# Kernel tuning notes

Measured on AMD Instinct MI355X. Metric: run time of the kernel, lower is better.

Reference implementation:

```python
import jax, jax.numpy as jnp
import numpy as np

B, D, H, O = 4096, 1024, 8192, 1000

def _l2norm_rows(w):
    return w / jnp.maximum(jnp.linalg.norm(w, axis=1, keepdims=True), 1e-12)

def setup_inputs() -> dict:
    key = jax.random.key(0)
    k1, k2, k3 = jax.random.split(key, 3)
    x = jax.random.normal(k1, (B, D), dtype=jnp.float32)
    kohonen_weights = _l2norm_rows(jax.random.normal(k2, (H, D), dtype=jnp.float32))
    grossberg_weights = _l2norm_rows(jax.random.normal(k3, (O, H), dtype=jnp.float32))
    return {"x": x, "kohonen_weights": kohonen_weights, "grossberg_weights": grossberg_weights}

def reference(x, kohonen_weights, grossberg_weights):
    # x: [B, D] (already flat), kohonen_weights: [H, D], grossberg_weights: [O, H]
    x2 = jnp.sum(x * x, axis=1, keepdims=True)              # [B, 1]
    w2 = jnp.sum(kohonen_weights * kohonen_weights, axis=1)  # [H]
    # Euclidean cdist via the expanded quadratic form (same as torch.cdist p=2)
    sq = x2 + w2[None, :] - 2.0 * (x @ kohonen_weights.T)    # [B, H]
    distances = jnp.sqrt(jnp.maximum(sq, 0.0))
    winners = jnp.argmin(distances, axis=1)                  # [B] int
    # one_hot @ grossberg_weights.T is exactly a row gather of grossberg_weights.T
    output = jnp.take(grossberg_weights.T, winners, axis=0)  # [B, O]
    return (output, winners)
```

## Files before the change

### kernel.cpp

```cpp
#include <hip/hip_runtime.h>
#include <hip/hip_bf16.h>
#include <hip/hip_fp16.h>


#define BB 4096
#define DD 1024
#define HH 8192
#define OO 1000

#define BM 128
#define BN 128
#define BK 64
#define NITER (DD / BK)
#define NTILES (HH / BN)
#define SA_TILE (BM * BK)
#define SB_TILE (BN * BK)

typedef _Float16 f16;
typedef float f32x16 __attribute__((ext_vector_type(16)));
typedef int v8i __attribute__((ext_vector_type(8)));
typedef int v4i __attribute__((ext_vector_type(4)));
union Frag { v8i v; v4i h[2]; };

typedef __attribute__((address_space(3))) uint32_t lds_u32_t;
typedef __attribute__((address_space(1))) uint32_t glb_u32_t;

__device__ __forceinline__ uint32_t packkey(float v, int col) {
  uint32_t u = __float_as_uint(v);
  uint32_t mask = (uint32_t)((int32_t)u >> 31) | 0x80000000u;
  u ^= mask;
  return (u & 0xFFFFFF80u) | (uint32_t)col;
}
__device__ __forceinline__ float unpackval(uint32_t k) {
  uint32_t u = k & 0xFFFFFF80u;
  uint32_t mask = (k & 0x80000000u) ? 0x80000000u : 0xFFFFFFFFu;
  return __uint_as_float(u ^ mask);
}
__device__ __forceinline__ void kmerge(uint32_t& k1, uint32_t& k2,
                                       uint32_t o1, uint32_t o2) {
  uint32_t mn = min(k1, o1);
  uint32_t alt = (k1 > o1) ? k2 : o2;
  k1 = max(k1, o1);
  k2 = max(mn, alt);
}

__global__ __launch_bounds__(256) void cvt_kernel(
    const float* __restrict__ x, const float* __restrict__ kw,
    uint8_t* __restrict__ xq, uint8_t* __restrict__ kq,
    const float* __restrict__ G, float* __restrict__ Gt) {
  const int tid = threadIdx.x;
  const int blk = blockIdx.x;
  __shared__ float tile[32][33];
  if (blk < (BB + HH) / 4) {
#pragma unroll
    for (int i = 0; i < 4; ++i) {
      int r = blk * 4 + i;
      const float* src = (r < BB) ? (x + (size_t)r * DD)
                                  : (kw + (size_t)(r - BB) * DD);
      uint8_t* dst = (r < BB) ? (xq + (size_t)r * DD)
                              : (kq + (size_t)(r - BB) * DD);
      float4 v = ((const float4*)src)[tid];
      int p = 0;
      p = __builtin_amdgcn_cvt_pk_fp8_f32(v.x, v.y, p, false);
      p = __builtin_amdgcn_cvt_pk_fp8_f32(v.z, v.w, p, true);
      ((int*)dst)[tid] = p;
    }
  } else {
    if (Gt == nullptr) return;
    const int tb = blk - (BB + HH) / 4;
    const int tx = tid & 31;
    const int ty = tid >> 5;
#pragma unroll 1
    for (int j4 = 0; j4 < 4; ++j4) {
      int tile_id = tb * 4 + j4;
      int h0 = (tile_id >> 5) * 32;
      int o0 = (tile_id & 31) * 32;
      __syncthreads();
#pragma unroll
      for (int j = 0; j < 4; ++j) {
        int o = o0 + ty + j * 8;
        if (o < OO) tile[ty + j * 8][tx] = G[(size_t)o * HH + h0 + tx];
      }
      __syncthreads();
#pragma unroll
      for (int j = 0; j < 4; ++j) {
        int o = o0 + tx;
        int h = h0 + ty + j * 8;
        if (o < OO) Gt[(size_t)h * OO + o] = tile[tx][ty + j * 8];
      }
    }
  }
}

__global__ __launch_bounds__(256, 3) void gemm_top2(
    const uint8_t* __restrict__ A, const uint8_t* __restrict__ Bt,
    uint4* __restrict__ pk) {
  __shared__ __align__(16) uint8_t sA[2][SA_TILE];
  __shared__ __align__(16) uint8_t sB[2][SB_TILE];
  __shared__ uint2 mk[BM][2];

  const int tid = threadIdx.x;
  const int w = tid >> 6;
  const int L = tid & 63;

  const int bid = blockIdx.y * gridDim.x + blockIdx.x;
  const int c8 = bid & 7;
  const int tt = bid >> 3;
  const int nx = c8 * 8 + (tt & 7);
  const int my = tt >> 3;
  const int m0 = my * BM;
  const int n0 = nx * BN;

  const int wr = w >> 1;
  const int wc = w & 1;

  f32x16 acc[2][2];
#pragma unroll
  for (int i = 0; i < 2; ++i)
#pragma unroll
    for (int j = 0; j < 2; ++j)
#pragma unroll
      for (int q = 0; q < 16; ++q) acc[i][j][q] = 0.f;

  const int l31 = L & 31;
  const int kh = L >> 5;

  const uint8_t* pA[2]; int dA[2];
  const uint8_t* pB[2]; int dB[2];
#pragma unroll
  for (int j = 0; j < 2; ++j) {
    int c = tid + 256 * j;
    int r = c >> 2;
    int so = ((c & 3) ^ ((r >> 1) & 3)) * 16;
    pA[j] = A + (size_t)(m0 + r) * DD + so;
    pB[j] = Bt + (size_t)(n0 + r) * DD + so;
    dA[j] = c * 16;
    dB[j] = c * 16;
  }

  auto stage = [&](int t, int p) {
#pragma unroll
    for (int j = 0; j < 2; ++j)
      __builtin_amdgcn_global_load_lds((const glb_u32_t*)(pA[j] + (size_t)t * BK),
                                       (lds_u32_t*)(&sA[p][0] + dA[j]), 16, 0, 0);
#pragma unroll
    for (int j = 0; j < 2; ++j)
      __builtin_amdgcn_global_load_lds((const glb_u32_t*)(pB[j] + (size_t)t * BK),
                                       (lds_u32_t*)(&sB[p][0] + dB[j]), 16, 0, 0);
  };

  const int t2 = (l31 >> 1) & 3;
  const int off_lo = ((2 * kh) ^ t2) * 16;
  const int off_hi = ((2 * kh + 1) ^ t2) * 16;
  const int raBase = (wr * 64 + l31) * BK;
  const int rbBase = (wc * 64 + l31) * BK;

  stage(0, 0);

#pragma unroll 1
  for (int kt = 0; kt < NITER; ++kt) {
    asm volatile("s_waitcnt lgkmcnt(0)" ::: "memory");
    __builtin_amdgcn_s_barrier();
    asm volatile("" ::: "memory");

    if (kt < NITER - 1) {
      stage(kt + 1, (kt + 1) & 1);
      asm volatile("s_waitcnt vmcnt(4)" ::: "memory");
    } else {
      asm volatile("s_waitcnt vmcnt(0)" ::: "memory");
    }

    const uint8_t* bufA = &sA[kt & 1][0];
    const uint8_t* bufB = &sB[kt & 1][0];

    __builtin_amdgcn_s_setprio(1);
    Frag af[2], bf[2];
#pragma unroll
    for (int j = 0; j < 2; ++j) {
      const uint8_t* base = bufA + raBase + j * 32 * BK;
      af[j].h[0] = *(const v4i*)(base + off_lo);
      af[j].h[1] = *(const v4i*)(base + off_hi);
    }
#pragma unroll
    for (int i = 0; i < 2; ++i) {
      const uint8_t* base = bufB + rbBase + i * 32 * BK;
      bf[i].h[0] = *(const v4i*)(base + off_lo);
      bf[i].h[1] = *(const v4i*)(base + off_hi);
    }
#pragma unroll
    for (int i = 0; i < 2; ++i)
#pragma unroll
      for (int j = 0; j < 2; ++j)
        acc[i][j] = __builtin_amdgcn_mfma_scale_f32_32x32x64_f8f6f4(
            bf[i].v, af[j].v, acc[i][j],
            0 , 0 ,
            0, 0x7F7F7F7Fu , 0, 0x7F7F7F7Fu);
    __builtin_amdgcn_s_setprio(0);
  }

#pragma unroll
  for (int j = 0; j < 2; ++j) {
    uint32_t k1 = 0, k2 = 0;
#pragma unroll
    for (int i = 0; i < 2; ++i) {
#pragma unroll
      for (int q = 0; q < 16; ++q) {
        int hcol = wc * 64 + i * 32 + (q & 3) + 8 * (q >> 2) + 4 * kh;
        uint32_t kj = packkey(acc[i][j][q], hcol);
        if (kj > k1) { k2 = k1; k1 = kj; }
        else k2 = max(k2, kj);
      }
    }
    uint32_t o1 = (uint32_t)__shfl_xor((int)k1, 32, 64);
    uint32_t o2 = (uint32_t)__shfl_xor((int)k2, 32, 64);
    kmerge(k1, k2, o1, o2);
    if (kh == 0) mk[wr * 64 + j * 32 + l31][wc] = make_uint2(k1, k2);
  }
  __syncthreads();
  if (tid < BM) {
    uint2 a = mk[tid][0], b = mk[tid][1];
    pk[(size_t)(m0 + tid) * NTILES + nx] = make_uint4(a.x, a.y, b.x, b.y);
  }
}

__global__ __launch_bounds__(256) void select_kernel(
    const float* __restrict__ x, const float* __restrict__ kw,
    const uint4* __restrict__ pk,
    const float* __restrict__ Gt, const float* __restrict__ G,
    float* __restrict__ out, float* __restrict__ out_w) {
  const int b = blockIdx.x * 4 + (threadIdx.x >> 6);
  const int L = threadIdx.x & 63;

  const float4* x4 = (const float4*)(x + (size_t)b * DD);
  float4 xv[4];
#pragma unroll
  for (int j = 0; j < 4; ++j) xv[j] = x4[L + 64 * j];

  uint4 kp = pk[(size_t)b * NTILES + L];

  double x2 = 0.0;
#pragma unroll
  for (int j = 0; j < 4; ++j)
    x2 += (double)xv[j].x * xv[j].x + (double)xv[j].y * xv[j].y +
          (double)xv[j].z * xv[j].z + (double)xv[j].w * xv[j].w;
#pragma unroll
  for (int msk = 1; msk < 64; msk <<= 1) x2 += __shfl_xor(x2, msk, 64);

  uint32_t m = max(kp.x, kp.z);
#pragma unroll
  for (int msk = 1; msk < 64; msk <<= 1)
    m = max(m, (uint32_t)__shfl_xor((int)m, msk, 64));
  const uint32_t thrk = packkey(unpackval(m) - 0.35f, 0);

  unsigned long long cand[4];
  cand[0] = __ballot(kp.x >= thrk);
  cand[1] = __ballot(kp.y >= thrk);
  cand[2] = __ballot(kp.z >= thrk);
  cand[3] = __ballot(kp.w >= thrk);

  double best = 1e300;
  int bestc = 0x7fffffff;
#pragma unroll 1
  for (int pass = 0; pass < 4; ++pass) {
    unsigned long long bits = cand[pass];
    uint32_t mykey = (pass == 0) ? kp.x : (pass == 1) ? kp.y
                    : (pass == 2) ? kp.z : kp.w;
    while (bits) {
      int tt = __ffsll((long long)bits) - 1;
      bits &= bits - 1;
      uint32_t kbt = (uint32_t)__shfl((int)mykey, tt, 64);
      int col = tt * 128 + (int)(kbt & 127u);
      const float4* k4 = (const float4*)(kw + (size_t)col * DD);
      double dot = 0.0, w2 = 0.0;
#pragma unroll
      for (int j = 0; j < 4; ++j) {
        float4 wv = k4[L + 64 * j];
        dot += (double)xv[j].x * wv.x + (double)xv[j].y * wv.y +
               (double)xv[j].z * wv.z + (double)xv[j].w * wv.w;
        w2 += (double)wv.x * wv.x + (double)wv.y * wv.y +
              (double)wv.z * wv.z + (double)wv.w * wv.w;
      }
#pragma unroll
      for (int msk = 1; msk < 64; msk <<= 1) {
        dot += __shfl_xor(dot, msk, 64);
        w2 += __shfl_xor(w2, msk, 64);
      }
      double sq = x2 + w2 - 2.0 * dot;
      if (sq < best || (sq == best && col < bestc)) { best = sq; bestc = col; }
    }
  }

  if (L == 0) out_w[b] = (float)bestc;
  if (Gt != nullptr) {
    const float4* gsrc = (const float4*)(Gt + (size_t)bestc * OO);
    float4* gdst = (float4*)(out + (size_t)b * OO);
#pragma unroll
    for (int j = 0; j < 4; ++j) {
      int q = L + 64 * j;
      if (q < OO / 4) gdst[q] = gsrc[q];
    }
  } else {
#pragma unroll 1
    for (int j = 0; j < 16; ++j) {
      int o = L + 64 * j;
      if (o < OO) out[(size_t)b * OO + o] = G[(size_t)o * HH + bestc];
    }
  }
}

extern "C" void kernel_launch(void* const* d_in, const int* in_sizes, int n_in,
                              void* d_out, int out_size, void* d_ws, size_t ws_size,
                              hipStream_t stream) {
  const float* x  = (const float*)d_in[0];
  const float* kw = (const float*)d_in[1];
  const float* gw = (const float*)d_in[2];
  float* out = (float*)d_out;
  float* out_w = out + (size_t)BB * OO;

  const size_t MB = 1024 * 1024;
  char* ws = (char*)d_ws;
  uint8_t* xq = (uint8_t*)(ws);
  uint8_t* kq = (uint8_t*)(ws + 4 * MB);
  uint4*   pk = (uint4*)(ws + 12 * MB);
  float*   Gt = (float*)(ws + 16 * MB);
  const size_t need = 16 * MB + sizeof(float) * (size_t)HH * OO;
  float* GtArg = (ws_size >= need) ? Gt : nullptr;

  int cvt_blocks = (BB + HH) / 4 + (GtArg ? 2048 : 0);
  cvt_kernel<<<cvt_blocks, 256, 0, stream>>>(x, kw, xq, kq, gw, GtArg);

  dim3 g(HH / BN, BB / BM);
  gemm_top2<<<g, 256, 0, stream>>>(xq, kq, pk);

  select_kernel<<<BB / 4, 256, 0, stream>>>(x, kw, pk, GtArg, gw, out, out_w);
}
```

Measured before the change: 200.4 us.

## Overlap Grossberg transpose with GEMM blocks and triple-buffer LDS staging

Moves the G transpose out of the conversion kernel and into the GEMM launch. Odd block IDs perform the transpose and even ones run the GEMM, so the memory-bound transpose runs alongside the compute-bound MFMA work. The GEMM mainloop also goes from double to triple buffering, prefetching two K-steps ahead to hide global-to-LDS latency. The larger LDS footprint (3 stages) may reduce occupancy below the launch-bounds target, and the interleaved transpose blocks take up scheduling slots.

```diff
diff --git a/kernel.cpp b/kernel.cpp
--- a/kernel.cpp
+++ b/kernel.cpp
@@ -13,6 +13,7 @@
 #define BK 64
 #define NITER (DD / BK)
 #define NTILES (HH / BN)
+#define NGEMM ((BB / BM) * (HH / BN))
 #define SA_TILE (BM * BK)
 #define SB_TILE (BN * BK)
 
@@ -46,66 +47,73 @@
 
 __global__ __launch_bounds__(256) void cvt_kernel(
     const float* __restrict__ x, const float* __restrict__ kw,
-    uint8_t* __restrict__ xq, uint8_t* __restrict__ kq,
-    const float* __restrict__ G, float* __restrict__ Gt) {
+    uint8_t* __restrict__ xq, uint8_t* __restrict__ kq) {
   const int tid = threadIdx.x;
   const int blk = blockIdx.x;
-  __shared__ float tile[32][33];
-  if (blk < (BB + HH) / 4) {
-#pragma unroll
-    for (int i = 0; i < 4; ++i) {
-      int r = blk * 4 + i;
-      const float* src = (r < BB) ? (x + (size_t)r * DD)
-                                  : (kw + (size_t)(r - BB) * DD);
-      uint8_t* dst = (r < BB) ? (xq + (size_t)r * DD)
-                              : (kq + (size_t)(r - BB) * DD);
-      float4 v = ((const float4*)src)[tid];
-      int p = 0;
-      p = __builtin_amdgcn_cvt_pk_fp8_f32(v.x, v.y, p, false);
-      p = __builtin_amdgcn_cvt_pk_fp8_f32(v.z, v.w, p, true);
-      ((int*)dst)[tid] = p;
-    }
-  } else {
-    if (Gt == nullptr) return;
-    const int tb = blk - (BB + HH) / 4;
-    const int tx = tid & 31;
-    const int ty = tid >> 5;
-#pragma unroll 1
-    for (int j4 = 0; j4 < 4; ++j4) {
-      int tile_id = tb * 4 + j4;
-      int h0 = (tile_id >> 5) * 32;
-      int o0 = (tile_id & 31) * 32;
-      __syncthreads();
-#pragma unroll
-      for (int j = 0; j < 4; ++j) {
-        int o = o0 + ty + j * 8;
-        if (o < OO) tile[ty + j * 8][tx] = G[(size_t)o * HH + h0 + tx];
-      }
-      __syncthreads();
-#pragma unroll
-      for (int j = 0; j < 4; ++j) {
-        int o = o0 + tx;
-        int h = h0 + ty + j * 8;
-        if (o < OO) Gt[(size_t)h * OO + o] = tile[tx][ty + j * 8];
-      }
-    }
+#pragma unroll
+  for (int i = 0; i < 4; ++i) {
+    int r = blk * 4 + i;
+    const float* src = (r < BB) ? (x + (size_t)r * DD)
+                                : (kw + (size_t)(r - BB) * DD);
+    uint8_t* dst = (r < BB) ? (xq + (size_t)r * DD)
+                            : (kq + (size_t)(r - BB) * DD);
+    float4 v = ((const float4*)src)[tid];
+    int p = 0;
+    p = __builtin_amdgcn_cvt_pk_fp8_f32(v.x, v.y, p, false);
+    p = __builtin_amdgcn_cvt_pk_fp8_f32(v.z, v.w, p, true);
+    ((int*)dst)[tid] = p;
   }
 }
 
 __global__ __launch_bounds__(256, 3) void gemm_top2(
     const uint8_t* __restrict__ A, const uint8_t* __restrict__ Bt,
-    uint4* __restrict__ pk) {
-  __shared__ __align__(16) uint8_t sA[2][SA_TILE];
-  __shared__ __align__(16) uint8_t sB[2][SB_TILE];
+    uint4* __restrict__ pk,
+    const float* __restrict__ G, float* __restrict__ Gt) {
+  __shared__ __align__(16) uint8_t sA[3][SA_TILE];
+  __shared__ __align__(16) uint8_t sB[3][SB_TILE];
   __shared__ uint2 mk[BM][2];
 
   const int tid = threadIdx.x;
+  const int bid0 = blockIdx.x;
+
+  int gid;
+  if (gridDim.x > NGEMM) {
+    if (bid0 & 1) {
+      float (*tile)[33] = (float(*)[33])&sA[0][0];
+      const int tb = bid0 >> 1;
+      const int tx = tid & 31;
+      const int ty = tid >> 5;
+#pragma unroll 1
+      for (int j4 = 0; j4 < 4; ++j4) {
+        int tile_id = tb * 4 + j4;
+        int h0 = (tile_id >> 5) * 32;
+        int o0 = (tile_id & 31) * 32;
+        __syncthreads();
+#pragma unroll
+        for (int j = 0; j < 4; ++j) {
+          int o = o0 + ty + j * 8;
+          if (o < OO) tile[ty + j * 8][tx] = G[(size_t)o * HH + h0 + tx];
+        }
+        __syncthreads();
+#pragma unroll
+        for (int j = 0; j < 4; ++j) {
+          int o = o0 + tx;
+          int h = h0 + ty + j * 8;
+          if (o < OO) Gt[(size_t)h * OO + o] = tile[tx][ty + j * 8];
+        }
+      }
+      return;
+    }
+    gid = bid0 >> 1;
+  } else {
+    gid = bid0;
+  }
+
   const int w = tid >> 6;
   const int L = tid & 63;
 
-  const int bid = blockIdx.y * gridDim.x + blockIdx.x;
-  const int c8 = bid & 7;
-  const int tt = bid >> 3;
+  const int c8 = gid & 7;
+  const int tt = gid >> 3;
   const int nx = c8 * 8 + (tt & 7);
   const int my = tt >> 3;
   const int m0 = my * BM;
@@ -156,22 +164,25 @@
   const int rbBase = (wc * 64 + l31) * BK;
 
   stage(0, 0);
-
+  stage(1, 1);
+
+  int cur = 0;
 #pragma unroll 1
   for (int kt = 0; kt < NITER; ++kt) {
-    asm volatile("s_waitcnt lgkmcnt(0)" ::: "memory");
+    if (kt == NITER - 1)
+      asm volatile("s_waitcnt vmcnt(0) lgkmcnt(0)" ::: "memory");
+    else
+      asm volatile("s_waitcnt vmcnt(4) lgkmcnt(0)" ::: "memory");
     __builtin_amdgcn_s_barrier();
     asm volatile("" ::: "memory");
 
-    if (kt < NITER - 1) {
-      stage(kt + 1, (kt + 1) & 1);
-      asm volatile("s_waitcnt vmcnt(4)" ::: "memory");
-    } else {
-      asm volatile("s_waitcnt vmcnt(0)" ::: "memory");
-    }
-
-    const uint8_t* bufA = &sA[kt & 1][0];
-    const uint8_t* bufB = &sB[kt & 1][0];
+    if (kt + 2 < NITER) {
+      int stp = cur + 2; if (stp >= 3) stp -= 3;
+      stage(kt + 2, stp);
+    }
+
+    const uint8_t* bufA = &sA[cur][0];
+    const uint8_t* bufB = &sB[cur][0];
 
     __builtin_amdgcn_s_setprio(1);
     Frag af[2], bf[2];
@@ -196,6 +207,8 @@
             0 , 0 ,
             0, 0x7F7F7F7Fu , 0, 0x7F7F7F7Fu);
     __builtin_amdgcn_s_setprio(0);
+
+    cur = (cur == 2) ? 0 : cur + 1;
   }
 
 #pragma unroll
@@ -326,11 +339,10 @@
   const size_t need = 16 * MB + sizeof(float) * (size_t)HH * OO;
   float* GtArg = (ws_size >= need) ? Gt : nullptr;
 
-  int cvt_blocks = (BB + HH) / 4 + (GtArg ? 2048 : 0);
-  cvt_kernel<<<cvt_blocks, 256, 0, stream>>>(x, kw, xq, kq, gw, GtArg);
-
-  dim3 g(HH / BN, BB / BM);
-  gemm_top2<<<g, 256, 0, stream>>>(xq, kq, pk);
+  cvt_kernel<<<(BB + HH) / 4, 256, 0, stream>>>(x, kw, xq, kq);
+
+  int gblocks = NGEMM + (GtArg ? NGEMM : 0);
+  gemm_top2<<<gblocks, 256, 0, stream>>>(xq, kq, pk, gw, GtArg);
 
   select_kernel<<<BB / 4, 256, 0, stream>>>(x, kw, pk, GtArg, gw, out, out_w);
 }
```

New measurement: 221.2 us. +10.4%, slower.
